# Kernel optimization log

Hardware: AMD Instinct MI355X
Metric: run time of the kernel (lower is better)

## Reference

```python
import jax, jax.numpy as jnp
import numpy as np

N = 40000      # n_nodes
E = 640000     # n_edges (avg degree 16)
D = 128        # hidden_dim
L = 4          # n_layers
EPS = 1e-6     # equinox RMSNorm default eps


def setup_inputs() -> dict:
    key = jax.random.key(0)
    ks = jax.random.split(key, 11)
    s = 1.0 / np.sqrt(D)
    return {
        "x": jax.random.normal(ks[0], (N, D), jnp.float32),
        "e": jax.random.randint(ks[1], (E, 2), 0, N, dtype=jnp.int32),
        # conv layers (stacked over L, matching eqx.filter_vmap construction)
        "Wc": jax.random.normal(ks[2], (L, D, D), jnp.float32) * s,
        "bc": jax.random.normal(ks[3], (L, D), jnp.float32) * s,
        "gc": jnp.ones((L, D), jnp.float32),   # RMSNorm weight
        "bgc": jnp.zeros((L, D), jnp.float32),  # RMSNorm bias
        # hidden layers
        "Wh": jax.random.normal(ks[4], (L, D, D), jnp.float32) * s,
        "bh": jax.random.normal(ks[5], (L, D), jnp.float32) * s,
        "gh": jnp.ones((L, D), jnp.float32),
        "bgh": jnp.zeros((L, D), jnp.float32),
    }


def _rmsnorm(h, g, b):
    return h * jax.lax.rsqrt(jnp.mean(h * h, axis=-1, keepdims=True) + EPS) * g + b


def reference(x, e, Wc, bc, gc, bgc, Wh, bh, gh, bgh):
    src, dst = e[:, 0], e[:, 1]

    def step(h, params):
        W, b, g, bg, W2, b2, g2, bg2 = params
        # --- GConvLayerEdges ---
        m = jax.nn.relu(jnp.einsum('ed,od->eo', h[src], W) + b)   # [E, D]
        # degree (segment_sum of ones_like(m) in original; all columns equal)
        deg = jax.ops.segment_sum(jnp.ones((E, 1), h.dtype), dst, num_segments=N)
        mm = jax.ops.segment_max(m, dst, num_segments=N)          # [N, D]
        mm = jnp.where(deg == 0, 0.0, mm)
        h = _rmsnorm(h + mm, g, bg)
        # --- HiddenLayer ---
        y = jax.nn.relu(jnp.einsum('nd,od->no', h, W2) + b2)
        h = _rmsnorm(h + y, g2, bg2)
        return h, None

    out, _ = jax.lax.scan(step, x, (Wc, bc, gc, bgc, Wh, bh, gh, bgh))
    return out
```

## Files before the change

kernel.cpp:

```cpp
#include <hip/hip_runtime.h>
#include <hip/hip_bf16.h>
#include <stdint.h>
#include <string.h>

#define NN 40000
#define NE 640000
#define D  128
#define NL 4
#define EPSV 1e-6f
#define CSRP 960000

typedef __attribute__((ext_vector_type(8))) short          s16x8;
typedef __attribute__((ext_vector_type(8))) unsigned short u16x8;
typedef __attribute__((ext_vector_type(4))) unsigned short u16x4;
typedef __attribute__((ext_vector_type(2))) unsigned short u16x2;
typedef __attribute__((ext_vector_type(4))) float          f32x4;

static __device__ __forceinline__ unsigned short f2b_bits(float f) {
  uint32_t u = __float_as_uint(f);
  uint32_t r = (u + 0x7fffu + ((u >> 16) & 1u)) >> 16;
  return (unsigned short)r;
}
static __device__ __forceinline__ float b2f(unsigned short b) {
  return __uint_as_float((uint32_t)b << 16);
}
static __device__ __forceinline__ u16x2 pmax(u16x2 x, u16x2 y) {
  return __builtin_elementwise_max(x, y);
}

__global__ void k_prep(const float* __restrict__ Wc, const float* __restrict__ Wh,
                       unsigned short* __restrict__ wcb, unsigned short* __restrict__ whb) {
  int i = blockIdx.x * 256 + threadIdx.x;
  if (i < NL * D * D) {
    wcb[i] = f2b_bits(Wc[i]);
    whb[i] = f2b_bits(Wh[i]);
  }
}

__global__ void k_init(int* __restrict__ csr, unsigned short* __restrict__ s0,
                       unsigned short* __restrict__ s1) {
  int i = blockIdx.x * 256 + threadIdx.x;
  if (i < CSRP) csr[i] = NN;
  if (i < D) { s0[i] = 0; s1[i] = 0; }
}

__global__ void k_count(const int* __restrict__ e, int* __restrict__ deg) {
  int i = blockIdx.x * 256 + threadIdx.x;
  if (i < NE) atomicAdd(&deg[e[2 * i + 1]], 1);
}

__global__ void k_alloc(const int* __restrict__ deg, int* __restrict__ total,
                        int* __restrict__ rs) {
  int i = blockIdx.x * 256 + threadIdx.x;
  if (i < NN) rs[i] = atomicAdd(total, (deg[i] + 7) & ~7);
}

__global__ void k_fill(const int* __restrict__ e, const int* __restrict__ rs,
                       int* __restrict__ cursor, int* __restrict__ csr) {
  int i = blockIdx.x * 256 + threadIdx.x;
  if (i < NE) {
    int s = e[2 * i + 0];
    int d = e[2 * i + 1];
    int p = atomicAdd(&cursor[d], 1);
    csr[rs[d] + p] = s;
  }
}

__global__ __launch_bounds__(256) void k_gemm0(
    const float* __restrict__ hin,
    const unsigned short* __restrict__ Wb,
    const float* __restrict__ bias,
    unsigned short* __restrict__ tout) {
  __shared__ float lds[4][16][D];
  int wave = threadIdx.x >> 6, lane = threadIdx.x & 63;
  int rowbase = (blockIdx.x * 4 + wave) * 16;
  int c15 = lane & 15, grp = lane >> 4;

  s16x8 a[4];
  {
    const float* hp = hin + (size_t)(rowbase + c15) * D;
#pragma unroll
    for (int ks = 0; ks < 4; ++ks) {
      int k0 = ks * 32 + grp * 8;
      f32x4 x0 = *(const f32x4*)(hp + k0);
      f32x4 x1 = *(const f32x4*)(hp + k0 + 4);
      u16x8 av;
      av[0] = f2b_bits(x0[0]); av[1] = f2b_bits(x0[1]);
      av[2] = f2b_bits(x0[2]); av[3] = f2b_bits(x0[3]);
      av[4] = f2b_bits(x1[0]); av[5] = f2b_bits(x1[1]);
      av[6] = f2b_bits(x1[2]); av[7] = f2b_bits(x1[3]);
      a[ks] = __builtin_bit_cast(s16x8, av);
    }
  }

  f32x4 acc[8];
#pragma unroll
  for (int ct = 0; ct < 8; ++ct) { f32x4 z = {0.f, 0.f, 0.f, 0.f}; acc[ct] = z; }
#pragma unroll
  for (int ct = 0; ct < 8; ++ct) {
    const unsigned short* wp = Wb + (size_t)(ct * 16 + c15) * D;
#pragma unroll
    for (int ks = 0; ks < 4; ++ks) {
      s16x8 b = *(const s16x8*)(wp + ks * 32 + grp * 8);
      acc[ct] = __builtin_amdgcn_mfma_f32_16x16x32_bf16(a[ks], b, acc[ct], 0, 0, 0);
    }
  }
#pragma unroll
  for (int ct = 0; ct < 8; ++ct) {
    int col = ct * 16 + c15;
    float bv = bias[col];
#pragma unroll
    for (int r = 0; r < 4; ++r)
      lds[wave][grp * 4 + r][col] = fmaxf(acc[ct][r] + bv, 0.f);
  }
  __syncthreads();
#pragma unroll
  for (int it = 0; it < 4; ++it) {
    int idx = it * 512 + lane * 8;
    int r = idx >> 7, c = idx & 127;
    const float* lp = &lds[wave][r][c];
    f32x4 v0 = *(const f32x4*)lp;
    f32x4 v1 = *(const f32x4*)(lp + 4);
    u16x8 ov;
    ov[0] = f2b_bits(v0[0]); ov[1] = f2b_bits(v0[1]);
    ov[2] = f2b_bits(v0[2]); ov[3] = f2b_bits(v0[3]);
    ov[4] = f2b_bits(v1[0]); ov[5] = f2b_bits(v1[1]);
    ov[6] = f2b_bits(v1[2]); ov[7] = f2b_bits(v1[3]);
    *(u16x8*)(tout + (size_t)(rowbase + r) * D + c) = ov;
  }
}

template <int WRITE_T>
__global__ __launch_bounds__(512) void k_layer(
    const float* __restrict__ hin,
    const uint32_t* __restrict__ tp,
    const int* __restrict__ rs, const int* __restrict__ deg, const int* __restrict__ csr,
    const float* __restrict__ gcv, const float* __restrict__ bgcv,
    const unsigned short* __restrict__ Whb, const float* __restrict__ bhv,
    const float* __restrict__ ghv, const float* __restrict__ bghv,
    const unsigned short* __restrict__ Wcb, const float* __restrict__ bcv,
    float* __restrict__ hout, unsigned short* __restrict__ tout) {
  __shared__ float u[16][132];
  int tid = threadIdx.x;
  int wave = tid >> 6, lane = tid & 63;
  int q = lane & 15, g = lane >> 4;
  int rowbase = blockIdx.x * 16;

  {
    int waveu = __builtin_amdgcn_readfirstlane(wave);
    int na = rowbase + waveu * 2;
    int r0a = rs[na], r0b = rs[na + 1];
    int dpa = (deg[na] + 7) & ~7;
    int dpb = (deg[na + 1] + 7) & ~7;
    const char* __restrict__ tb = (const char*)tp;
    uint32_t loff = (uint32_t)lane * 4u;
    int d0 = lane * 2;

    float2 hva  = *(const float2*)(hin + (size_t)na * D + d0);
    float2 hvb  = *(const float2*)(hin + (size_t)(na + 1) * D + d0);
    float2 gc2  = *(const float2*)(gcv + d0);
    float2 bgc2 = *(const float2*)(bgcv + d0);

    const int* __restrict__ csa = csr + r0a;
    const int* __restrict__ csb = csr + r0b;

#define TL(S) (*(const uint32_t*)((tb + (((uint32_t)(S)) << 8)) + loff))
    u16x2 a0 = {0,0}, a1 = {0,0}, a2 = {0,0}, a3 = {0,0};
    for (int i = 0; i < dpa; i += 8) {
      uint32_t q0 = TL(csa[i+0]), q1 = TL(csa[i+1]), q2 = TL(csa[i+2]), q3 = TL(csa[i+3]);
      uint32_t q4 = TL(csa[i+4]), q5 = TL(csa[i+5]), q6 = TL(csa[i+6]), q7 = TL(csa[i+7]);
      a0 = pmax(a0, __builtin_bit_cast(u16x2, q0));
      a1 = pmax(a1, __builtin_bit_cast(u16x2, q1));
      a2 = pmax(a2, __builtin_bit_cast(u16x2, q2));
      a3 = pmax(a3, __builtin_bit_cast(u16x2, q3));
      a0 = pmax(a0, __builtin_bit_cast(u16x2, q4));
      a1 = pmax(a1, __builtin_bit_cast(u16x2, q5));
      a2 = pmax(a2, __builtin_bit_cast(u16x2, q6));
      a3 = pmax(a3, __builtin_bit_cast(u16x2, q7));
    }
    u16x2 b0 = {0,0}, b1 = {0,0}, b2 = {0,0}, b3 = {0,0};
    for (int i = 0; i < dpb; i += 8) {
      uint32_t q0 = TL(csb[i+0]), q1 = TL(csb[i+1]), q2 = TL(csb[i+2]), q3 = TL(csb[i+3]);
      uint32_t q4 = TL(csb[i+4]), q5 = TL(csb[i+5]), q6 = TL(csb[i+6]), q7 = TL(csb[i+7]);
      b0 = pmax(b0, __builtin_bit_cast(u16x2, q0));
      b1 = pmax(b1, __builtin_bit_cast(u16x2, q1));
      b2 = pmax(b2, __builtin_bit_cast(u16x2, q2));
      b3 = pmax(b3, __builtin_bit_cast(u16x2, q3));
      b0 = pmax(b0, __builtin_bit_cast(u16x2, q4));
      b1 = pmax(b1, __builtin_bit_cast(u16x2, q5));
      b2 = pmax(b2, __builtin_bit_cast(u16x2, q6));
      b3 = pmax(b3, __builtin_bit_cast(u16x2, q7));
    }
#undef TL
    u16x2 am = pmax(pmax(a0, a1), pmax(a2, a3));
    u16x2 bm = pmax(pmax(b0, b1), pmax(b2, b3));

    float ua0 = hva.x + b2f(am[0]);
    float ua1 = hva.y + b2f(am[1]);
    float ub0 = hvb.x + b2f(bm[0]);
    float ub1 = hvb.y + b2f(bm[1]);
    float ssa = ua0 * ua0 + ua1 * ua1;
    float ssb = ub0 * ub0 + ub1 * ub1;
#pragma unroll
    for (int off = 32; off; off >>= 1) {
      ssa += __shfl_xor(ssa, off);
      ssb += __shfl_xor(ssb, off);
    }
    float rfa = rsqrtf(ssa * (1.f / D) + EPSV);
    float rfb = rsqrtf(ssb * (1.f / D) + EPSV);
    int nla = waveu * 2;
    u[nla][d0]         = ua0 * rfa * gc2.x + bgc2.x;
    u[nla][d0 + 1]     = ua1 * rfa * gc2.y + bgc2.y;
    u[nla + 1][d0]     = ub0 * rfb * gc2.x + bgc2.x;
    u[nla + 1][d0 + 1] = ub1 * rfb * gc2.y + bgc2.y;
  }
  __syncthreads();

  const char* whB = (const char*)Whb;
  uint32_t wrow = (uint32_t)(wave * 16 + q) * (D * 2);
  s16x8 a[4];
#pragma unroll
  for (int ks = 0; ks < 4; ++ks) {
    int k0 = ks * 32 + g * 8;
    f32x4 x0 = *(const f32x4*)&u[q][k0];
    f32x4 x1 = *(const f32x4*)&u[q][k0 + 4];
    u16x8 av;
    av[0] = f2b_bits(x0[0]); av[1] = f2b_bits(x0[1]);
    av[2] = f2b_bits(x0[2]); av[3] = f2b_bits(x0[3]);
    av[4] = f2b_bits(x1[0]); av[5] = f2b_bits(x1[1]);
    av[6] = f2b_bits(x1[2]); av[7] = f2b_bits(x1[3]);
    a[ks] = __builtin_bit_cast(s16x8, av);
  }
  f32x4 acc = {0.f, 0.f, 0.f, 0.f};
#pragma unroll
  for (int ks = 0; ks < 4; ++ks) {
    s16x8 b = *(const s16x8*)(whB + wrow + (uint32_t)(ks * 32 + g * 8) * 2);
    acc = __builtin_amdgcn_mfma_f32_16x16x32_bf16(a[ks], b, acc, 0, 0, 0);
  }
  __syncthreads();
  {
    int col = wave * 16 + q;
    float bv = bhv[col];
#pragma unroll
    for (int r = 0; r < 4; ++r)
      u[g * 4 + r][col] += fmaxf(acc[r] + bv, 0.f);
  }
  __syncthreads();
  {
    int d0 = lane * 2;
    float2 gh2  = *(const float2*)(ghv + d0);
    float2 bgh2 = *(const float2*)(bghv + d0);
#pragma unroll
    for (int j = 0; j < 2; ++j) {
      int r = wave * 2 + j;
      float u0 = u[r][d0], u1 = u[r][d0 + 1];
      float ss = u0 * u0 + u1 * u1;
#pragma unroll
      for (int off2 = 32; off2; off2 >>= 1) ss += __shfl_xor(ss, off2);
      float rf = rsqrtf(ss * (1.f / D) + EPSV);
      float o0 = u0 * rf * gh2.x + bgh2.x;
      float o1 = u1 * rf * gh2.y + bgh2.y;
      u[r][d0]     = o0;
      u[r][d0 + 1] = o1;
      float2 o; o.x = o0; o.y = o1;
      *(float2*)(hout + (size_t)(rowbase + r) * D + d0) = o;
    }
  }

  if (WRITE_T) {
    __syncthreads();
    const char* wcB = (const char*)Wcb;
    s16x8 a2[4];
#pragma unroll
    for (int ks = 0; ks < 4; ++ks) {
      int k0 = ks * 32 + g * 8;
      f32x4 x0 = *(const f32x4*)&u[q][k0];
      f32x4 x1 = *(const f32x4*)&u[q][k0 + 4];
      u16x8 av;
      av[0] = f2b_bits(x0[0]); av[1] = f2b_bits(x0[1]);
      av[2] = f2b_bits(x0[2]); av[3] = f2b_bits(x0[3]);
      av[4] = f2b_bits(x1[0]); av[5] = f2b_bits(x1[1]);
      av[6] = f2b_bits(x1[2]); av[7] = f2b_bits(x1[3]);
      a2[ks] = __builtin_bit_cast(s16x8, av);
    }
    f32x4 acc2 = {0.f, 0.f, 0.f, 0.f};
#pragma unroll
    for (int ks = 0; ks < 4; ++ks) {
      s16x8 b = *(const s16x8*)(wcB + wrow + (uint32_t)(ks * 32 + g * 8) * 2);
      acc2 = __builtin_amdgcn_mfma_f32_16x16x32_bf16(a2[ks], b, acc2, 0, 0, 0);
    }
    __syncthreads();
    {
      int col = wave * 16 + q;
      float bv = bcv[col];
#pragma unroll
      for (int r = 0; r < 4; ++r)
        u[g * 4 + r][col] = fmaxf(acc2[r] + bv, 0.f);
    }
    __syncthreads();
    {
      int r = tid >> 5, c = (tid & 31) * 4;
      f32x4 v = *(const f32x4*)&u[r][c];
      u16x4 ov;
      ov[0] = f2b_bits(v[0]); ov[1] = f2b_bits(v[1]);
      ov[2] = f2b_bits(v[2]); ov[3] = f2b_bits(v[3]);
      *(u16x4*)(tout + (size_t)(rowbase + r) * D + c) = ov;
    }
  }
}

extern "C" void kernel_launch(void* const* d_in, const int* in_sizes, int n_in,
                              void* d_out, int out_size, void* d_ws, size_t ws_size,
                              hipStream_t stream) {
  (void)in_sizes; (void)n_in; (void)out_size; (void)ws_size;
  const float* x   = (const float*)d_in[0];
  const int*   e   = (const int*)d_in[1];
  const float* Wc  = (const float*)d_in[2];
  const float* bc  = (const float*)d_in[3];
  const float* gc  = (const float*)d_in[4];
  const float* bgc = (const float*)d_in[5];
  const float* Wh  = (const float*)d_in[6];
  const float* bh  = (const float*)d_in[7];
  const float* gh  = (const float*)d_in[8];
  const float* bgh = (const float*)d_in[9];
  float* out = (float*)d_out;

  char* base = (char*)d_ws;
  unsigned short* t0  = (unsigned short*)(base + 0);
  unsigned short* t1  = (unsigned short*)(base + 10240512);
  float*          hA  = (float*)(base + 20481024);
  unsigned short* wcb = (unsigned short*)(base + 40961024);
  unsigned short* whb = (unsigned short*)(base + 41092096);
  int*            deg = (int*)(base + 41223168);
  int*            cur = (int*)(base + 41383168);
  int*            tot = (int*)(base + 41543168);
  int*            rs  = (int*)(base + 41543232);
  int*            csr = (int*)(base + 41703232);

  k_prep<<<512, 256, 0, stream>>>(Wc, Wh, wcb, whb);
  hipMemsetAsync(deg, 0, 2 * 160000 + 64, stream);
  k_init<<<3750, 256, 0, stream>>>(csr, t0 + (size_t)NN * D, t1 + (size_t)NN * D);
  k_count<<<2500, 256, 0, stream>>>(e, deg);
  k_alloc<<<157, 256, 0, stream>>>(deg, tot, rs);
  k_fill<<<2500, 256, 0, stream>>>(e, rs, cur, csr);

  k_gemm0<<<625, 256, 0, stream>>>(x, wcb, bc, t0);

  unsigned short* tbuf[2] = {t0, t1};
  for (int l = 0; l < NL; ++l) {
    const float* hin = (l == 0) ? x : hA;
    const uint32_t* tin = (const uint32_t*)tbuf[l & 1];
    if (l < NL - 1) {
      k_layer<1><<<2500, 512, 0, stream>>>(
          hin, tin, rs, deg, csr,
          gc + l * D, bgc + l * D,
          whb + (size_t)l * D * D, bh + l * D, gh + l * D, bgh + l * D,
          wcb + (size_t)(l + 1) * D * D, bc + (l + 1) * D,
          hA, tbuf[(l + 1) & 1]);
    } else {
      k_layer<0><<<2500, 512, 0, stream>>>(
          hin, tin, rs, deg, csr,
          gc + l * D, bgc + l * D,
          whb + (size_t)l * D * D, bh + l * D, gh + l * D, bgh + l * D,
          nullptr, nullptr,
          out, nullptr);
    }
  }
}
```

Before: 268.3 us.

## Split message tensor into four column planes for segment-max gather

The bf16 message tensor t is stored as four planes of 32 columns each (64 bytes per row) instead of one 256-byte row. The gather now has 8 lanes read 8 bytes each from 8 different edges at once, and loops over the 4 planes. Lane partial maxima are then reduced with shuffles and passed through shared memory before the RMSNorm. The aim is better locality per plane and fewer loads in flight per edge. The cost is more loop iterations, extra shuffle reductions and an LDS round trip.

```diff
diff --git a/kernel.cpp b/kernel.cpp
--- a/kernel.cpp
+++ b/kernel.cpp
@@ -9,6 +9,8 @@
 #define NL 4
 #define EPSV 1e-6f
 #define CSRP 960000
+#define PLANE_ELEMS 1280032
+#define PLANE_BYTES 2560064
 
 typedef __attribute__((ext_vector_type(8))) short          s16x8;
 typedef __attribute__((ext_vector_type(8))) unsigned short u16x8;
@@ -24,8 +26,10 @@
 static __device__ __forceinline__ float b2f(unsigned short b) {
   return __uint_as_float((uint32_t)b << 16);
 }
-static __device__ __forceinline__ u16x2 pmax(u16x2 x, u16x2 y) {
-  return __builtin_elementwise_max(x, y);
+static __device__ __forceinline__ uint32_t pk32(uint32_t a, uint32_t b) {
+  u16x2 x = __builtin_bit_cast(u16x2, a);
+  u16x2 y = __builtin_bit_cast(u16x2, b);
+  return __builtin_bit_cast(uint32_t, __builtin_elementwise_max(x, y));
 }
 
 __global__ void k_prep(const float* __restrict__ Wc, const float* __restrict__ Wh,
@@ -37,11 +41,16 @@
   }
 }
 
-__global__ void k_init(int* __restrict__ csr, unsigned short* __restrict__ s0,
-                       unsigned short* __restrict__ s1) {
+__global__ void k_init(int* __restrict__ csr, unsigned short* __restrict__ t0,
+                       unsigned short* __restrict__ t1) {
   int i = blockIdx.x * 256 + threadIdx.x;
   if (i < CSRP) csr[i] = NN;
-  if (i < D) { s0[i] = 0; s1[i] = 0; }
+  if (i < 128) {
+    int p = i >> 5, j = i & 31;
+    size_t off = (size_t)p * PLANE_ELEMS + (size_t)NN * 32 + j;
+    t0[off] = 0;
+    t1[off] = 0;
+  }
 }
 
 __global__ void k_count(const int* __restrict__ e, int* __restrict__ deg) {
@@ -126,14 +135,15 @@
     ov[2] = f2b_bits(v0[2]); ov[3] = f2b_bits(v0[3]);
     ov[4] = f2b_bits(v1[0]); ov[5] = f2b_bits(v1[1]);
     ov[6] = f2b_bits(v1[2]); ov[7] = f2b_bits(v1[3]);
-    *(u16x8*)(tout + (size_t)(rowbase + r) * D + c) = ov;
+    int p = c >> 5, co = c & 31;
+    *(u16x8*)(tout + (size_t)p * PLANE_ELEMS + (size_t)(rowbase + r) * 32 + co) = ov;
   }
 }
 
 template <int WRITE_T>
 __global__ __launch_bounds__(512) void k_layer(
     const float* __restrict__ hin,
-    const uint32_t* __restrict__ tp,
+    const unsigned short* __restrict__ tp,
     const int* __restrict__ rs, const int* __restrict__ deg, const int* __restrict__ csr,
     const float* __restrict__ gcv, const float* __restrict__ bgcv,
     const unsigned short* __restrict__ Whb, const float* __restrict__ bhv,
@@ -141,6 +151,7 @@
     const unsigned short* __restrict__ Wcb, const float* __restrict__ bcv,
     float* __restrict__ hout, unsigned short* __restrict__ tout) {
   __shared__ float u[16][132];
+  __shared__ uint2 mld[16][33];
   int tid = threadIdx.x;
   int wave = tid >> 6, lane = tid & 63;
   int q = lane & 15, g = lane >> 4;
@@ -152,53 +163,58 @@
     int r0a = rs[na], r0b = rs[na + 1];
     int dpa = (deg[na] + 7) & ~7;
     int dpb = (deg[na + 1] + 7) & ~7;
-    const char* __restrict__ tb = (const char*)tp;
-    uint32_t loff = (uint32_t)lane * 4u;
+    int eg = lane >> 3;
+    uint32_t go = (uint32_t)(lane & 7) * 8u;
     int d0 = lane * 2;
+    int nla = waveu * 2;
 
     float2 hva  = *(const float2*)(hin + (size_t)na * D + d0);
     float2 hvb  = *(const float2*)(hin + (size_t)(na + 1) * D + d0);
     float2 gc2  = *(const float2*)(gcv + d0);
     float2 bgc2 = *(const float2*)(bgcv + d0);
 
-    const int* __restrict__ csa = csr + r0a;
-    const int* __restrict__ csb = csr + r0b;
-
-#define TL(S) (*(const uint32_t*)((tb + (((uint32_t)(S)) << 8)) + loff))
-    u16x2 a0 = {0,0}, a1 = {0,0}, a2 = {0,0}, a3 = {0,0};
-    for (int i = 0; i < dpa; i += 8) {
-      uint32_t q0 = TL(csa[i+0]), q1 = TL(csa[i+1]), q2 = TL(csa[i+2]), q3 = TL(csa[i+3]);
-      uint32_t q4 = TL(csa[i+4]), q5 = TL(csa[i+5]), q6 = TL(csa[i+6]), q7 = TL(csa[i+7]);
-      a0 = pmax(a0, __builtin_bit_cast(u16x2, q0));
-      a1 = pmax(a1, __builtin_bit_cast(u16x2, q1));
-      a2 = pmax(a2, __builtin_bit_cast(u16x2, q2));
-      a3 = pmax(a3, __builtin_bit_cast(u16x2, q3));
-      a0 = pmax(a0, __builtin_bit_cast(u16x2, q4));
-      a1 = pmax(a1, __builtin_bit_cast(u16x2, q5));
-      a2 = pmax(a2, __builtin_bit_cast(u16x2, q6));
-      a3 = pmax(a3, __builtin_bit_cast(u16x2, q7));
-    }
-    u16x2 b0 = {0,0}, b1 = {0,0}, b2 = {0,0}, b3 = {0,0};
-    for (int i = 0; i < dpb; i += 8) {
-      uint32_t q0 = TL(csb[i+0]), q1 = TL(csb[i+1]), q2 = TL(csb[i+2]), q3 = TL(csb[i+3]);
-      uint32_t q4 = TL(csb[i+4]), q5 = TL(csb[i+5]), q6 = TL(csb[i+6]), q7 = TL(csb[i+7]);
-      b0 = pmax(b0, __builtin_bit_cast(u16x2, q0));
-      b1 = pmax(b1, __builtin_bit_cast(u16x2, q1));
-      b2 = pmax(b2, __builtin_bit_cast(u16x2, q2));
-      b3 = pmax(b3, __builtin_bit_cast(u16x2, q3));
-      b0 = pmax(b0, __builtin_bit_cast(u16x2, q4));
-      b1 = pmax(b1, __builtin_bit_cast(u16x2, q5));
-      b2 = pmax(b2, __builtin_bit_cast(u16x2, q6));
-      b3 = pmax(b3, __builtin_bit_cast(u16x2, q7));
-    }
-#undef TL
-    u16x2 am = pmax(pmax(a0, a1), pmax(a2, a3));
-    u16x2 bm = pmax(pmax(b0, b1), pmax(b2, b3));
-
-    float ua0 = hva.x + b2f(am[0]);
-    float ua1 = hva.y + b2f(am[1]);
-    float ub0 = hvb.x + b2f(bm[0]);
-    float ub1 = hvb.y + b2f(bm[1]);
+    const char* tb = (const char*)tp;
+    int rmax = dpa > dpb ? dpa : dpb;
+
+#pragma unroll
+    for (int p = 0; p < 4; ++p) {
+      const char* pb = tb + (size_t)p * PLANE_BYTES;
+      u16x4 ma = {0, 0, 0, 0}, mb = {0, 0, 0, 0};
+      for (int i = 0; i < rmax; i += 8) {
+        if (i < dpa) {
+          uint32_t s = (uint32_t)csr[r0a + i + eg];
+          u16x4 v = *(const u16x4*)(pb + ((s << 6) + go));
+          ma = __builtin_elementwise_max(ma, v);
+        }
+        if (i < dpb) {
+          uint32_t s = (uint32_t)csr[r0b + i + eg];
+          u16x4 v = *(const u16x4*)(pb + ((s << 6) + go));
+          mb = __builtin_elementwise_max(mb, v);
+        }
+      }
+      uint2 ra = __builtin_bit_cast(uint2, ma);
+      uint2 rb = __builtin_bit_cast(uint2, mb);
+#pragma unroll
+      for (int mk = 8; mk <= 32; mk <<= 1) {
+        ra.x = pk32(ra.x, (uint32_t)__shfl_xor((int)ra.x, mk));
+        ra.y = pk32(ra.y, (uint32_t)__shfl_xor((int)ra.y, mk));
+        rb.x = pk32(rb.x, (uint32_t)__shfl_xor((int)rb.x, mk));
+        rb.y = pk32(rb.y, (uint32_t)__shfl_xor((int)rb.y, mk));
+      }
+      if (lane < 8) {
+        mld[nla][p * 8 + lane]     = ra;
+        mld[nla + 1][p * 8 + lane] = rb;
+      }
+    }
+
+    uint2 qa = mld[nla][lane >> 1];
+    uint2 qb = mld[nla + 1][lane >> 1];
+    uint32_t pa = (lane & 1) ? qa.y : qa.x;
+    uint32_t pbv = (lane & 1) ? qb.y : qb.x;
+    float ua0 = hva.x + b2f((unsigned short)(pa & 0xffffu));
+    float ua1 = hva.y + b2f((unsigned short)(pa >> 16));
+    float ub0 = hvb.x + b2f((unsigned short)(pbv & 0xffffu));
+    float ub1 = hvb.y + b2f((unsigned short)(pbv >> 16));
     float ssa = ua0 * ua0 + ua1 * ua1;
     float ssb = ub0 * ub0 + ub1 * ub1;
 #pragma unroll
@@ -208,7 +224,6 @@
     }
     float rfa = rsqrtf(ssa * (1.f / D) + EPSV);
     float rfb = rsqrtf(ssb * (1.f / D) + EPSV);
-    int nla = waveu * 2;
     u[nla][d0]         = ua0 * rfa * gc2.x + bgc2.x;
     u[nla][d0 + 1]     = ua1 * rfa * gc2.y + bgc2.y;
     u[nla + 1][d0]     = ub0 * rfb * gc2.x + bgc2.x;
@@ -304,7 +319,8 @@
       u16x4 ov;
       ov[0] = f2b_bits(v[0]); ov[1] = f2b_bits(v[1]);
       ov[2] = f2b_bits(v[2]); ov[3] = f2b_bits(v[3]);
-      *(u16x4*)(tout + (size_t)(rowbase + r) * D + c) = ov;
+      int p = c >> 5, co = c & 31;
+      *(u16x4*)(tout + (size_t)p * PLANE_ELEMS + (size_t)(rowbase + r) * 32 + co) = ov;
     }
   }
 }
@@ -339,7 +355,7 @@
 
   k_prep<<<512, 256, 0, stream>>>(Wc, Wh, wcb, whb);
   hipMemsetAsync(deg, 0, 2 * 160000 + 64, stream);
-  k_init<<<3750, 256, 0, stream>>>(csr, t0 + (size_t)NN * D, t1 + (size_t)NN * D);
+  k_init<<<3750, 256, 0, stream>>>(csr, t0, t1);
   k_count<<<2500, 256, 0, stream>>>(e, deg);
   k_alloc<<<157, 256, 0, stream>>>(deg, tot, rs);
   k_fill<<<2500, 256, 0, stream>>>(e, rs, cur, csr);
@@ -349,7 +365,7 @@
   unsigned short* tbuf[2] = {t0, t1};
   for (int l = 0; l < NL; ++l) {
     const float* hin = (l == 0) ? x : hA;
-    const uint32_t* tin = (const uint32_t*)tbuf[l & 1];
+    const unsigned short* tin = tbuf[l & 1];
     if (l < NL - 1) {
       k_layer<1><<<2500, 512, 0, stream>>>(
           hin, tin, rs, deg, csr,
```

After: 393.7 us. 46.8% more time.
